# Performance work log

Measured on AMD Instinct MI355X. Metric: run time of the kernel, lower is better.

The kernel has to match this reference:

```python
import jax, jax.numpy as jnp
import numpy as np

N = 50000      # num_nodes
E = 800000     # num_edges (before self loops)
EMB = 128      # emb_dim
GH = 64        # gcn_hidden
TD = 4         # temporal_dim
B = 64         # batch of sequences
T = 200        # max sequence length
H = 128        # lstm_hidden (per direction)
IN_DIM = 2 + EMB + TD


def lstm_scan(x_tbi, w_ih, w_hh, b_ih, b_hh):
    """x_tbi: [T, B, I] -> hidden states [T, B, H]. PyTorch gate order i,f,g,o."""
    Bsz = x_tbi.shape[1]
    Hh = w_hh.shape[1]

    def step(carry, xt):
        h, c = carry
        g = xt @ w_ih.T + h @ w_hh.T + b_ih + b_hh
        i, f, gg, o = jnp.split(g, 4, axis=-1)
        c = jax.nn.sigmoid(f) * c + jax.nn.sigmoid(i) * jnp.tanh(gg)
        h = jax.nn.sigmoid(o) * jnp.tanh(c)
        return (h, c), h

    init = (jnp.zeros((Bsz, Hh), x_tbi.dtype), jnp.zeros((Bsz, Hh), x_tbi.dtype))
    _, hs = jax.lax.scan(step, init, x_tbi)
    return hs


def gcn_layer(x, W, b, src, dst, ew):
    """PyG GCNConv: linear -> symmetric-norm gather/scatter-add -> bias.
    (self loops already appended to src/dst/ew by caller)"""
    h = x @ W  # [N, out]
    deg = jax.ops.segment_sum(ew, dst, num_segments=N)
    dinv = jnp.where(deg > 0, jax.lax.rsqrt(deg), 0.0)
    norm = dinv[src] * ew * dinv[dst]            # [E+N]
    msg = h[src] * norm[:, None]                  # gather + scale
    return jax.ops.segment_sum(msg, dst, num_segments=N) + b


def setup_inputs() -> dict:
    key = jax.random.key(0)
    ks = jax.random.split(key, 16)
    s = 0.02
    return {
        'x_coords': jax.random.normal(ks[0], (N, 2), jnp.float32),
        'temporal_features': jax.random.uniform(ks[1], (N, TD), jnp.float32, -1.0, 1.0),
        'edge_index': jax.random.randint(ks[2], (2, E), 0, N),
        'edge_weight': jnp.ones((E,), jnp.float32),
        'seq': jax.random.randint(ks[3], (B, T), 0, N),
        'lengths': jax.random.randint(ks[4], (B,), 1, T + 1),
        'node_emb': jax.random.normal(ks[5], (N, EMB), jnp.float32) * s,
        'gcn1_w': jax.random.normal(ks[6], (IN_DIM, GH), jnp.float32) * s,
        'gcn1_b': jnp.zeros((GH,), jnp.float32),
        'gcn2_w': jax.random.normal(ks[7], (GH, EMB), jnp.float32) * s,
        'gcn2_b': jnp.zeros((EMB,), jnp.float32),
        'w_ih_f': jax.random.normal(ks[8], (4 * H, EMB), jnp.float32) * s,
        'w_hh_f': jax.random.normal(ks[9], (4 * H, H), jnp.float32) * s,
        'b_ih_f': jnp.zeros((4 * H,), jnp.float32),
        'b_hh_f': jnp.zeros((4 * H,), jnp.float32),
        'w_ih_b': jax.random.normal(ks[10], (4 * H, EMB), jnp.float32) * s,
        'w_hh_b': jax.random.normal(ks[11], (4 * H, H), jnp.float32) * s,
        'b_ih_b': jnp.zeros((4 * H,), jnp.float32),
        'b_hh_b': jnp.zeros((4 * H,), jnp.float32),
        'attn_w': jax.random.normal(ks[12], (2 * H,), jnp.float32) * s,
        'attn_b': jnp.zeros((), jnp.float32),
        'fc_w': jax.random.normal(ks[13], (2 * H, N), jnp.float32) * s,
        'fc_b': jnp.zeros((N,), jnp.float32),
    }


def reference(x_coords, temporal_features, edge_index, edge_weight, seq, lengths,
              node_emb, gcn1_w, gcn1_b, gcn2_w, gcn2_b,
              w_ih_f, w_hh_f, b_ih_f, b_hh_f,
              w_ih_b, w_hh_b, b_ih_b, b_hh_b,
              attn_w, attn_b, fc_w, fc_b):
    # --- GCN with self loops (PyG add_self_loops=True, fill_value=1) ---
    loop = jnp.arange(N)
    src = jnp.concatenate([edge_index[0], loop])
    dst = jnp.concatenate([edge_index[1], loop])
    ew = jnp.concatenate([edge_weight, jnp.ones((N,), edge_weight.dtype)])

    x = jnp.concatenate([x_coords, node_emb, temporal_features], axis=1)  # [N, 134]
    z = jax.nn.relu(gcn_layer(x, gcn1_w, gcn1_b, src, dst, ew))
    z = gcn_layer(z, gcn2_w, gcn2_b, src, dst, ew)  # dropout = identity (eval)

    # --- sequence embedding + BiLSTM ---
    seq_emb = z[seq]                                  # [B, T, EMB]
    h_f = lstm_scan(seq_emb.transpose(1, 0, 2), w_ih_f, w_hh_f, b_ih_f, b_hh_f)
    h_f = h_f.transpose(1, 0, 2)                      # [B, T, H]

    # backward direction: reverse each sequence within its valid length
    t = jnp.arange(T)
    valid = t[None, :] < lengths[:, None]             # [B, T]
    rev_idx = jnp.where(valid, lengths[:, None] - 1 - t[None, :], t[None, :])
    x_rev = jnp.take_along_axis(seq_emb, rev_idx[:, :, None], axis=1)
    h_b = lstm_scan(x_rev.transpose(1, 0, 2), w_ih_b, w_hh_b, b_ih_b, b_hh_b)
    h_b = jnp.take_along_axis(h_b.transpose(1, 0, 2), rev_idx[:, :, None], axis=1)

    lstm_out = jnp.concatenate([h_f, h_b], axis=-1)   # [B, T, 2H]

    # --- masked attention pooling ---
    scores = lstm_out @ attn_w + attn_b               # [B, T]
    scores = jnp.where(valid, scores, -jnp.inf)
    aw = jax.nn.softmax(scores, axis=1)
    context = jnp.einsum('bt,btd->bd', aw, lstm_out)  # [B, 2H]

    return context @ fc_w + fc_b                      # [B, N]
```

## Files before the change

kernel.cpp:

```cpp
#include <hip/hip_runtime.h>
#include <math.h>

#define NN 50000
#define NE 800000
#define EMB 128
#define GH 64
#define BB 64
#define TT 200
#define HH 128
#define G4 512
#define IND 134

__device__ __forceinline__ float sigf(float x) { return 1.0f / (1.0f + __expf(-x)); }
__device__ __forceinline__ float tanhf_(float x) { return 1.0f - 2.0f / (__expf(2.0f * x) + 1.0f); }
__device__ __forceinline__ void fma4(float4& a, float s, const float4 w) {
    a.x += s * w.x; a.y += s * w.y; a.z += s * w.z; a.w += s * w.w;
}

__global__ void hist_kernel(const int* __restrict__ ei, const float* __restrict__ ew,
                            int* __restrict__ cnt, float* __restrict__ degw) {
    int e = blockIdx.x * 256 + threadIdx.x;
    if (e >= NE) return;
    int d = ei[NE + e];
    atomicAdd(&cnt[d], 1);
    atomicAdd(&degw[d], ew[e]);
}

__global__ void dinv_kernel(const float* __restrict__ degw, float* __restrict__ dinv) {
    int n = blockIdx.x * 256 + threadIdx.x;
    if (n >= NN) return;
    dinv[n] = rsqrtf(degw[n] + 1.0f);
}

__global__ __launch_bounds__(1024) void scan1_kernel(const int* __restrict__ cnt,
                                                     int* __restrict__ rs, int* __restrict__ partials) {
    __shared__ int s[1024];
    int gid = blockIdx.x * 1024 + threadIdx.x;
    int v = (gid < NN) ? cnt[gid] : 0;
    s[threadIdx.x] = v;
    __syncthreads();
    for (int off = 1; off < 1024; off <<= 1) {
        int add = (threadIdx.x >= (unsigned)off) ? s[threadIdx.x - off] : 0;
        __syncthreads();
        s[threadIdx.x] += add;
        __syncthreads();
    }
    if (gid < NN) rs[gid] = s[threadIdx.x] - v;
    if (threadIdx.x == 1023) partials[blockIdx.x] = s[1023];
}

__global__ void scan2_kernel(int* __restrict__ partials, int nblk) {
    if (threadIdx.x == 0) {
        int acc = 0;
        for (int i = 0; i < nblk; ++i) { int v = partials[i]; partials[i] = acc; acc += v; }
    }
}

__global__ __launch_bounds__(1024) void scan3_kernel(const int* __restrict__ partials,
                                                     int* __restrict__ rs, int* __restrict__ cursor) {
    int gid = blockIdx.x * 1024 + threadIdx.x;
    if (gid < NN) {
        int v = rs[gid] + partials[gid >> 10];
        rs[gid] = v;
        cursor[gid] = v;
    }
    if (gid == 0) rs[NN] = NE;
}

__global__ void fill_kernel(const int* __restrict__ ei, const float* __restrict__ ew,
                            const float* __restrict__ dinv, int* __restrict__ cursor,
                            int* __restrict__ ssrc, float* __restrict__ sw) {
    int e = blockIdx.x * 256 + threadIdx.x;
    if (e >= NE) return;
    int s = ei[e], d = ei[NE + e];
    int pos = atomicAdd(&cursor[d], 1);
    ssrc[pos] = s;
    sw[pos] = ew[e] * dinv[s] * dinv[d];
}

__global__ __launch_bounds__(256) void gemm1_kernel(const float* __restrict__ coords,
                                                    const float* __restrict__ temporal,
                                                    const float* __restrict__ emb,
                                                    const float* __restrict__ W1,
                                                    float* __restrict__ h1) {
    __shared__ __align__(16) float wl[IND][GH];
    for (int i = threadIdx.x; i < IND * GH / 4; i += 256)
        ((float4*)wl)[i] = ((const float4*)W1)[i];
    __syncthreads();
    int n = blockIdx.x * 256 + threadIdx.x;
    if (n >= NN) return;
    float4 acc[16];
    float c0 = coords[2 * n], c1 = coords[2 * n + 1];
#pragma unroll
    for (int j = 0; j < 16; ++j) {
        float4 wa = *(const float4*)&wl[0][j * 4];
        float4 wb = *(const float4*)&wl[1][j * 4];
        float4 a;
        a.x = c0 * wa.x + c1 * wb.x; a.y = c0 * wa.y + c1 * wb.y;
        a.z = c0 * wa.z + c1 * wb.z; a.w = c0 * wa.w + c1 * wb.w;
        acc[j] = a;
    }
    const float4* er = (const float4*)(emb + (size_t)n * EMB);
#pragma unroll 2
    for (int k4 = 0; k4 < 32; ++k4) {
        float4 v = er[k4];
        int k = 2 + k4 * 4;
#pragma unroll
        for (int j = 0; j < 16; ++j) {
            fma4(acc[j], v.x, *(const float4*)&wl[k][j * 4]);
            fma4(acc[j], v.y, *(const float4*)&wl[k + 1][j * 4]);
            fma4(acc[j], v.z, *(const float4*)&wl[k + 2][j * 4]);
            fma4(acc[j], v.w, *(const float4*)&wl[k + 3][j * 4]);
        }
    }
    float t0 = temporal[4 * n], t1 = temporal[4 * n + 1], t2 = temporal[4 * n + 2], t3 = temporal[4 * n + 3];
#pragma unroll
    for (int j = 0; j < 16; ++j) {
        fma4(acc[j], t0, *(const float4*)&wl[130][j * 4]);
        fma4(acc[j], t1, *(const float4*)&wl[131][j * 4]);
        fma4(acc[j], t2, *(const float4*)&wl[132][j * 4]);
        fma4(acc[j], t3, *(const float4*)&wl[133][j * 4]);
        *(float4*)&h1[(size_t)n * GH + j * 4] = acc[j];
    }
}

__global__ __launch_bounds__(256) void agg_kernel(const float* __restrict__ hin,
                                                  const int* __restrict__ rs,
                                                  const int* __restrict__ ssrc,
                                                  const float* __restrict__ sw,
                                                  const float* __restrict__ dinv,
                                                  const float* __restrict__ bias, int relu,
                                                  float* __restrict__ hout) {
    int lane = threadIdx.x & 63;
    int wid = threadIdx.x >> 6;
    int n = blockIdx.x * 4 + wid;
    if (n >= NN) return;
    float dv = dinv[n];
    float acc = hin[(size_t)n * GH + lane] * (dv * dv);
    int i = rs[n], e1 = rs[n + 1];
    for (; i + 3 < e1; i += 4) {
        int s0 = ssrc[i], s1 = ssrc[i + 1], s2 = ssrc[i + 2], s3 = ssrc[i + 3];
        float w0 = sw[i], w1 = sw[i + 1], w2 = sw[i + 2], w3 = sw[i + 3];
        float a0 = hin[(size_t)s0 * GH + lane];
        float a1 = hin[(size_t)s1 * GH + lane];
        float a2 = hin[(size_t)s2 * GH + lane];
        float a3 = hin[(size_t)s3 * GH + lane];
        acc += a0 * w0 + a1 * w1 + a2 * w2 + a3 * w3;
    }
    for (; i < e1; ++i) acc += hin[(size_t)ssrc[i] * GH + lane] * sw[i];
    if (bias) acc += bias[lane];
    if (relu) acc = fmaxf(acc, 0.0f);
    hout[(size_t)n * GH + lane] = acc;
}

__global__ __launch_bounds__(256) void gemm2_kernel(const float* __restrict__ a2,
                                                    const float* __restrict__ W2,
                                                    const float* __restrict__ b2,
                                                    float* __restrict__ z2) {
    __shared__ __align__(16) float wl[GH][64];
    int j0 = blockIdx.y * 64;
    for (int i = threadIdx.x; i < GH * 16; i += 256) {
        int k = i >> 4, j4 = i & 15;
        *(float4*)&wl[k][j4 * 4] = *(const float4*)&W2[(size_t)k * EMB + j0 + j4 * 4];
    }
    __syncthreads();
    int n = blockIdx.x * 256 + threadIdx.x;
    if (n >= NN) return;
    float4 acc[16];
#pragma unroll
    for (int j = 0; j < 16; ++j) acc[j] = *(const float4*)&b2[j0 + j * 4];
    const float4* ar = (const float4*)(a2 + (size_t)n * GH);
#pragma unroll 2
    for (int k4 = 0; k4 < 16; ++k4) {
        float4 v = ar[k4];
        int k = k4 * 4;
#pragma unroll
        for (int j = 0; j < 16; ++j) {
            fma4(acc[j], v.x, *(const float4*)&wl[k][j * 4]);
            fma4(acc[j], v.y, *(const float4*)&wl[k + 1][j * 4]);
            fma4(acc[j], v.z, *(const float4*)&wl[k + 2][j * 4]);
            fma4(acc[j], v.w, *(const float4*)&wl[k + 3][j * 4]);
        }
    }
#pragma unroll
    for (int j = 0; j < 16; ++j)
        *(float4*)&z2[(size_t)n * EMB + j0 + j * 4] = acc[j];
}

__global__ void gather_kernel(const int* __restrict__ seq, const float* __restrict__ z2,
                              float* __restrict__ se) {
    int idx = blockIdx.x * 256 + threadIdx.x;
    if (idx >= BB * TT * 32) return;
    int r = idx >> 5, q = idx & 31;
    int node = seq[r];
    ((float4*)se)[(size_t)r * 32 + q] = ((const float4*)z2)[(size_t)node * 32 + q];
}

__global__ __launch_bounds__(256) void pregemm_kernel(const float* __restrict__ se,
                                                      const float* __restrict__ w_ih_f,
                                                      const float* __restrict__ w_ih_b,
                                                      const float* __restrict__ b_ih_f,
                                                      const float* __restrict__ b_hh_f,
                                                      const float* __restrict__ b_ih_b,
                                                      const float* __restrict__ b_hh_b,
                                                      const int* __restrict__ lengths,
                                                      float* __restrict__ xpf,
                                                      float* __restrict__ xpb) {
    int dir = blockIdx.z;
    const float* w_ih = dir ? w_ih_b : w_ih_f;
    int u0 = blockIdx.y * 64;
    __shared__ __align__(16) float wl[64][EMB];
    __shared__ float bs[64];
    {
        const float4* src = (const float4*)(w_ih + (size_t)u0 * EMB);
        for (int i = threadIdx.x; i < 64 * EMB / 4; i += 256) ((float4*)wl)[i] = src[i];
        if (threadIdx.x < 64) {
            int u = u0 + threadIdx.x;
            bs[threadIdx.x] = dir ? (b_ih_b[u] + b_hh_b[u]) : (b_ih_f[u] + b_hh_f[u]);
        }
    }
    __syncthreads();
    int m = blockIdx.x * 256 + threadIdx.x;
    if (m >= TT * BB) return;
    int t = m >> 6, b = m & 63;
    int tsrc = t;
    if (dir) {
        int len = lengths[b];
        if (t >= len) return;
        tsrc = len - 1 - t;
    }
    const float4* row = (const float4*)(se + ((size_t)b * TT + tsrc) * EMB);
    float accs[64];
#pragma unroll
    for (int j = 0; j < 64; ++j) accs[j] = bs[j];
#pragma unroll 2
    for (int k4 = 0; k4 < 32; ++k4) {
        float4 xv = row[k4];
#pragma unroll
        for (int j = 0; j < 64; ++j) {
            float4 wv = *(const float4*)&wl[j][k4 * 4];
            accs[j] += xv.x * wv.x + xv.y * wv.y + xv.z * wv.z + xv.w * wv.w;
        }
    }
    float* xp = dir ? xpb : xpf;
#pragma unroll
    for (int j4 = 0; j4 < 16; ++j4) {
        float4 o = make_float4(accs[j4 * 4], accs[j4 * 4 + 1], accs[j4 * 4 + 2], accs[j4 * 4 + 3]);
        *(float4*)&xp[(size_t)m * G4 + u0 + j4 * 4] = o;
    }
}

#define LSTM_LW(i) float4 W##i = wr[i]; \
    asm volatile("" : "+v"(W##i.x), "+v"(W##i.y), "+v"(W##i.z), "+v"(W##i.w));
#define LSTM_FMA(i) { float4 hv = h4[i]; \
    a0 += W##i.x * hv.x; a1 += W##i.y * hv.y; a2 += W##i.z * hv.z; a3 += W##i.w * hv.w; }

__global__ __launch_bounds__(512, 1) void lstm_kernel(const float* __restrict__ xpf,
                                                      const float* __restrict__ xpb,
                                                      const float* __restrict__ w_hh_f,
                                                      const float* __restrict__ w_hh_b,
                                                      const int* __restrict__ lengths,
                                                      float* __restrict__ hfo,
                                                      float* __restrict__ hbo) {
    int chain = blockIdx.x;
    int dir = chain & 1, b = chain >> 1;
    const float* w_hh = dir ? w_hh_b : w_hh_f;
    const float* xp = dir ? xpb : xpf;
    float* ho = dir ? hbo : hfo;
    int tid = threadIdx.x;
    int u = tid >> 2, g = tid & 3;
    int len = lengths[b];

    const float4* wr = (const float4*)(w_hh + (size_t)(g * HH + u) * HH);
    LSTM_LW(0) LSTM_LW(1) LSTM_LW(2) LSTM_LW(3) LSTM_LW(4) LSTM_LW(5) LSTM_LW(6) LSTM_LW(7)
    LSTM_LW(8) LSTM_LW(9) LSTM_LW(10) LSTM_LW(11) LSTM_LW(12) LSTM_LW(13) LSTM_LW(14) LSTM_LW(15)
    LSTM_LW(16) LSTM_LW(17) LSTM_LW(18) LSTM_LW(19) LSTM_LW(20) LSTM_LW(21) LSTM_LW(22) LSTM_LW(23)
    LSTM_LW(24) LSTM_LW(25) LSTM_LW(26) LSTM_LW(27) LSTM_LW(28) LSTM_LW(29) LSTM_LW(30) LSTM_LW(31)

    __shared__ __align__(16) float hl[2][HH];
    if (tid < HH) hl[0][tid] = 0.0f;
    __syncthreads();

    const float* xpt = xp + (size_t)b * G4 + g * HH + u;
    float cst = 0.0f;
    float xcur = xpt[0];
    for (int t = 0; t < len; ++t) {
        float xnext = (t + 1 < len) ? xpt[(size_t)(t + 1) * BB * G4] : 0.0f;
        const float4* h4 = (const float4*)hl[t & 1];
        float a0 = 0.0f, a1 = 0.0f, a2 = 0.0f, a3 = 0.0f;
        LSTM_FMA(0) LSTM_FMA(1) LSTM_FMA(2) LSTM_FMA(3) LSTM_FMA(4) LSTM_FMA(5) LSTM_FMA(6) LSTM_FMA(7)
        LSTM_FMA(8) LSTM_FMA(9) LSTM_FMA(10) LSTM_FMA(11) LSTM_FMA(12) LSTM_FMA(13) LSTM_FMA(14) LSTM_FMA(15)
        LSTM_FMA(16) LSTM_FMA(17) LSTM_FMA(18) LSTM_FMA(19) LSTM_FMA(20) LSTM_FMA(21) LSTM_FMA(22) LSTM_FMA(23)
        LSTM_FMA(24) LSTM_FMA(25) LSTM_FMA(26) LSTM_FMA(27) LSTM_FMA(28) LSTM_FMA(29) LSTM_FMA(30) LSTM_FMA(31)
        float acc = ((a0 + a1) + (a2 + a3)) + xcur;
        float a_own = (g == 2) ? tanhf_(acc) : sigf(acc);
        float sb = __shfl_xor(a_own, 1, 64);
        float sc = __shfl_xor(a_own, 2, 64);
        float sd = __shfl_xor(sb, 2, 64);
        float si = (g == 0) ? a_own : (g == 1) ? sb : (g == 2) ? sc : sd;
        float sf = (g == 0) ? sb : (g == 1) ? a_own : (g == 2) ? sd : sc;
        float sg = (g == 0) ? sc : (g == 1) ? sd : (g == 2) ? a_own : sb;
        float so = (g == 0) ? sd : (g == 1) ? sc : (g == 2) ? sb : a_own;
        cst = sf * cst + si * sg;
        float h = so * tanhf_(cst);
        if (g == 0) {
            hl[(t + 1) & 1][u] = h;
            int tt = dir ? (len - 1 - t) : t;
            ho[((size_t)b * TT + tt) * HH + u] = h;
        }
        __syncthreads();
        xcur = xnext;
    }
}

__global__ __launch_bounds__(256) void attn_kernel(const float* __restrict__ hf,
                                                   const float* __restrict__ hb,
                                                   const float* __restrict__ attn_w,
                                                   const float* __restrict__ attn_b,
                                                   const int* __restrict__ lengths,
                                                   float* __restrict__ ctx) {
    int b = blockIdx.x;
    int tid = threadIdx.x;
    int len = lengths[b];
    __shared__ __align__(16) float wl[256];
    __shared__ float pl[256];
    __shared__ float red[256];
    wl[tid] = attn_w[tid];
    __syncthreads();
    float sc = -3.0e38f;
    if (tid < len) {
        const float4* rf = (const float4*)(hf + ((size_t)b * TT + tid) * HH);
        const float4* rb = (const float4*)(hb + ((size_t)b * TT + tid) * HH);
        const float4* w4 = (const float4*)wl;
        float s = attn_b[0];
        for (int k4 = 0; k4 < 32; ++k4) {
            float4 a = rf[k4], ww = w4[k4];
            s += a.x * ww.x + a.y * ww.y + a.z * ww.z + a.w * ww.w;
        }
        for (int k4 = 0; k4 < 32; ++k4) {
            float4 a = rb[k4], ww = w4[32 + k4];
            s += a.x * ww.x + a.y * ww.y + a.z * ww.z + a.w * ww.w;
        }
        sc = s;
    }
    red[tid] = sc;
    __syncthreads();
    for (int off = 128; off > 0; off >>= 1) {
        if (tid < off) red[tid] = fmaxf(red[tid], red[tid + off]);
        __syncthreads();
    }
    float mx = red[0];
    __syncthreads();
    float e = (tid < len) ? __expf(sc - mx) : 0.0f;
    red[tid] = e;
    __syncthreads();
    for (int off = 128; off > 0; off >>= 1) {
        if (tid < off) red[tid] += red[tid + off];
        __syncthreads();
    }
    float inv = 1.0f / red[0];
    pl[tid] = e * inv;
    __syncthreads();
    float acc = 0.0f;
    const float* basep = (tid < HH) ? (hf + (size_t)b * TT * HH + tid)
                                    : (hb + (size_t)b * TT * HH + (tid - HH));
#pragma unroll 4
    for (int t = 0; t < len; ++t) acc += pl[t] * basep[(size_t)t * HH];
    ctx[(size_t)b * 256 + tid] = acc;
}

__global__ __launch_bounds__(256) void fc_kernel(const float* __restrict__ ctx,
                                                 const float* __restrict__ fc_w,
                                                 const float* __restrict__ fc_b,
                                                 float* __restrict__ out) {
    __shared__ __align__(16) float cl[64][256];
    for (int i = threadIdx.x; i < 64 * 256 / 4; i += 256)
        ((float4*)cl)[i] = ((const float4*)ctx)[i];
    __syncthreads();
    int nb = threadIdx.x & 63;
    int bq = threadIdx.x >> 6;
    int n = blockIdx.x * 64 + nb;
    if (n >= NN) return;
    float acc[16];
#pragma unroll
    for (int i = 0; i < 16; ++i) acc[i] = 0.0f;
#pragma unroll 2
    for (int k4 = 0; k4 < 64; ++k4) {
        int k = k4 * 4;
        float w0 = fc_w[(size_t)k * NN + n];
        float w1 = fc_w[(size_t)(k + 1) * NN + n];
        float w2 = fc_w[(size_t)(k + 2) * NN + n];
        float w3 = fc_w[(size_t)(k + 3) * NN + n];
#pragma unroll
        for (int i = 0; i < 16; ++i) {
            float4 cv = *(const float4*)&cl[bq * 16 + i][k];
            acc[i] += cv.x * w0 + cv.y * w1 + cv.z * w2 + cv.w * w3;
        }
    }
    float fb = fc_b[n];
#pragma unroll
    for (int i = 0; i < 16; ++i)
        out[(size_t)(bq * 16 + i) * NN + n] = acc[i] + fb;
}

extern "C" void kernel_launch(void* const* d_in, const int* in_sizes, int n_in,
                              void* d_out, int out_size, void* d_ws, size_t ws_size,
                              hipStream_t stream) {
    const float* x_coords   = (const float*)d_in[0];
    const float* temporal   = (const float*)d_in[1];
    const int*   edge_index = (const int*)d_in[2];
    const float* edge_w     = (const float*)d_in[3];
    const int*   seq        = (const int*)d_in[4];
    const int*   lengths    = (const int*)d_in[5];
    const float* node_emb   = (const float*)d_in[6];
    const float* gcn1_w     = (const float*)d_in[7];
    const float* gcn1_b     = (const float*)d_in[8];
    const float* gcn2_w     = (const float*)d_in[9];
    const float* gcn2_b     = (const float*)d_in[10];
    const float* w_ih_f     = (const float*)d_in[11];
    const float* w_hh_f     = (const float*)d_in[12];
    const float* b_ih_f     = (const float*)d_in[13];
    const float* b_hh_f     = (const float*)d_in[14];
    const float* w_ih_b     = (const float*)d_in[15];
    const float* w_hh_b     = (const float*)d_in[16];
    const float* b_ih_b     = (const float*)d_in[17];
    const float* b_hh_b     = (const float*)d_in[18];
    const float* attn_w     = (const float*)d_in[19];
    const float* attn_b     = (const float*)d_in[20];
    const float* fc_w       = (const float*)d_in[21];
    const float* fc_b       = (const float*)d_in[22];
    float* out = (float*)d_out;

    char* base = (char*)d_ws;
    size_t off = 0;
    auto alloc = [&](size_t nbytes) -> void* {
        void* p = base + off;
        off = (off + nbytes + 255) & ~(size_t)255;
        return p;
    };
    int*   cnt     = (int*)alloc((size_t)2 * NN * 4);
    float* degw    = (float*)(cnt + NN);
    float* dinv    = (float*)alloc((size_t)NN * 4);
    int*   rs      = (int*)alloc(((size_t)NN + 1) * 4);
    int*   cursor  = (int*)alloc((size_t)NN * 4);
    int*   partials= (int*)alloc(64 * 4);
    int*   ssrc    = (int*)alloc((size_t)NE * 4);
    float* sw      = (float*)alloc((size_t)NE * 4);
    float* h1      = (float*)alloc((size_t)NN * GH * 4);
    float* z1      = (float*)alloc((size_t)NN * GH * 4);
    float* a2      = h1;
    float* z2      = (float*)alloc((size_t)NN * EMB * 4);
    float* se      = (float*)alloc((size_t)BB * TT * EMB * 4);
    float* xpf     = (float*)alloc((size_t)TT * BB * G4 * 4);
    float* xpb     = (float*)alloc((size_t)TT * BB * G4 * 4);
    float* hfo     = (float*)alloc((size_t)BB * TT * HH * 4);
    float* hbo     = (float*)alloc((size_t)BB * TT * HH * 4);
    float* ctx     = (float*)alloc((size_t)BB * 256 * 4);
    (void)ws_size; (void)in_sizes; (void)n_in; (void)out_size;

    hipMemsetAsync(cnt, 0, (size_t)2 * NN * 4, stream);

    hist_kernel<<<(NE + 255) / 256, 256, 0, stream>>>(edge_index, edge_w, cnt, degw);
    dinv_kernel<<<(NN + 255) / 256, 256, 0, stream>>>(degw, dinv);
    const int nblk = (NN + 1023) / 1024;
    scan1_kernel<<<nblk, 1024, 0, stream>>>(cnt, rs, partials);
    scan2_kernel<<<1, 64, 0, stream>>>(partials, nblk);
    scan3_kernel<<<nblk, 1024, 0, stream>>>(partials, rs, cursor);
    fill_kernel<<<(NE + 255) / 256, 256, 0, stream>>>(edge_index, edge_w, dinv, cursor, ssrc, sw);

    gemm1_kernel<<<(NN + 255) / 256, 256, 0, stream>>>(x_coords, temporal, node_emb, gcn1_w, h1);
    agg_kernel<<<(NN + 3) / 4, 256, 0, stream>>>(h1, rs, ssrc, sw, dinv, gcn1_b, 1, z1);
    agg_kernel<<<(NN + 3) / 4, 256, 0, stream>>>(z1, rs, ssrc, sw, dinv, (const float*)nullptr, 0, a2);
    gemm2_kernel<<<dim3((NN + 255) / 256, 2), 256, 0, stream>>>(a2, gcn2_w, gcn2_b, z2);

    gather_kernel<<<(BB * TT * 32 + 255) / 256, 256, 0, stream>>>(seq, z2, se);
    pregemm_kernel<<<dim3(TT * BB / 256, 8, 2), 256, 0, stream>>>(
        se, w_ih_f, w_ih_b, b_ih_f, b_hh_f, b_ih_b, b_hh_b, lengths, xpf, xpb);
    lstm_kernel<<<BB * 2, 512, 0, stream>>>(xpf, xpb, w_hh_f, w_hh_b, lengths, hfo, hbo);
    attn_kernel<<<BB, 256, 0, stream>>>(hfo, hbo, attn_w, attn_b, lengths, ctx);
    fc_kernel<<<(NN + 63) / 64, 256, 0, stream>>>(ctx, fc_w, fc_b, out);
}
```

Baseline: 692.7 us.

## Split LSTM recurrent matvec over two thread halves and broadcast h via readlane

The recurrent kernel now uses 1024 threads per chain, with each half holding 64 of the 128 weight columns in registers, which halves the serial dot-product length per thread. The hidden-state vector is no longer read from LDS as float4 per step. Each lane loads one element and the values are broadcast with readlane. The two halves combine through a shared partial-sum buffer, which adds an extra barrier per timestep and leaves the second half idle during the gate nonlinearities.

```diff
diff --git a/kernel.cpp b/kernel.cpp
--- a/kernel.cpp
+++ b/kernel.cpp
@@ -15,6 +15,9 @@
 __device__ __forceinline__ float tanhf_(float x) { return 1.0f - 2.0f / (__expf(2.0f * x) + 1.0f); }
 __device__ __forceinline__ void fma4(float4& a, float s, const float4 w) {
     a.x += s * w.x; a.y += s * w.y; a.z += s * w.z; a.w += s * w.w;
+}
+__device__ __forceinline__ float rlf(float x, int k) {
+    return __int_as_float(__builtin_amdgcn_readlane(__float_as_int(x), k));
 }
 
 __global__ void hist_kernel(const int* __restrict__ ei, const float* __restrict__ ew,
@@ -252,61 +255,75 @@
 
 #define LSTM_LW(i) float4 W##i = wr[i]; \
     asm volatile("" : "+v"(W##i.x), "+v"(W##i.y), "+v"(W##i.z), "+v"(W##i.w));
-#define LSTM_FMA(i) { float4 hv = h4[i]; \
-    a0 += W##i.x * hv.x; a1 += W##i.y * hv.y; a2 += W##i.z * hv.z; a3 += W##i.w * hv.w; }
-
-__global__ __launch_bounds__(512, 1) void lstm_kernel(const float* __restrict__ xpf,
-                                                      const float* __restrict__ xpb,
-                                                      const float* __restrict__ w_hh_f,
-                                                      const float* __restrict__ w_hh_b,
-                                                      const int* __restrict__ lengths,
-                                                      float* __restrict__ hfo,
-                                                      float* __restrict__ hbo) {
+#define LSTM_RLFMA(i) { \
+    float s0 = rlf(hfrag, 4*i+0); a0 += s0 * W##i.x; \
+    float s1 = rlf(hfrag, 4*i+1); a1 += s1 * W##i.y; \
+    float s2 = rlf(hfrag, 4*i+2); a2 += s2 * W##i.z; \
+    float s3 = rlf(hfrag, 4*i+3); a3 += s3 * W##i.w; }
+
+__global__ __launch_bounds__(1024, 4) void lstm_kernel(const float* __restrict__ xpf,
+                                                       const float* __restrict__ xpb,
+                                                       const float* __restrict__ w_hh_f,
+                                                       const float* __restrict__ w_hh_b,
+                                                       const int* __restrict__ lengths,
+                                                       float* __restrict__ hfo,
+                                                       float* __restrict__ hbo) {
     int chain = blockIdx.x;
     int dir = chain & 1, b = chain >> 1;
     const float* w_hh = dir ? w_hh_b : w_hh_f;
     const float* xp = dir ? xpb : xpf;
     float* ho = dir ? hbo : hfo;
     int tid = threadIdx.x;
-    int u = tid >> 2, g = tid & 3;
+    int wv = tid >> 6;
+    int lam = tid & 63;
+    int p = wv >> 3;
+    int wj = wv & 7;
+    int j = wj * 64 + lam;
+    int g = lam & 3;
+    int u = j >> 2;
+    int r = g * HH + u;
     int len = lengths[b];
 
-    const float4* wr = (const float4*)(w_hh + (size_t)(g * HH + u) * HH);
+    const float4* wr = (const float4*)(w_hh + (size_t)r * HH + p * 64);
     LSTM_LW(0) LSTM_LW(1) LSTM_LW(2) LSTM_LW(3) LSTM_LW(4) LSTM_LW(5) LSTM_LW(6) LSTM_LW(7)
     LSTM_LW(8) LSTM_LW(9) LSTM_LW(10) LSTM_LW(11) LSTM_LW(12) LSTM_LW(13) LSTM_LW(14) LSTM_LW(15)
-    LSTM_LW(16) LSTM_LW(17) LSTM_LW(18) LSTM_LW(19) LSTM_LW(20) LSTM_LW(21) LSTM_LW(22) LSTM_LW(23)
-    LSTM_LW(24) LSTM_LW(25) LSTM_LW(26) LSTM_LW(27) LSTM_LW(28) LSTM_LW(29) LSTM_LW(30) LSTM_LW(31)
-
-    __shared__ __align__(16) float hl[2][HH];
-    if (tid < HH) hl[0][tid] = 0.0f;
-    __syncthreads();
-
-    const float* xpt = xp + (size_t)b * G4 + g * HH + u;
+
+    __shared__ float hl[HH];
+    __shared__ float part[G4];
+    if (tid < HH) hl[tid] = 0.0f;
+    __syncthreads();
+
+    const float* xpt = xp + (size_t)b * G4 + r;
     float cst = 0.0f;
-    float xcur = xpt[0];
+    float xcur = (p == 0) ? xpt[0] : 0.0f;
     for (int t = 0; t < len; ++t) {
-        float xnext = (t + 1 < len) ? xpt[(size_t)(t + 1) * BB * G4] : 0.0f;
-        const float4* h4 = (const float4*)hl[t & 1];
+        float hfrag = hl[(p << 6) + lam];
+        float xnext = (p == 0 && t + 1 < len) ? xpt[(size_t)(t + 1) * (BB * G4)] : 0.0f;
         float a0 = 0.0f, a1 = 0.0f, a2 = 0.0f, a3 = 0.0f;
-        LSTM_FMA(0) LSTM_FMA(1) LSTM_FMA(2) LSTM_FMA(3) LSTM_FMA(4) LSTM_FMA(5) LSTM_FMA(6) LSTM_FMA(7)
-        LSTM_FMA(8) LSTM_FMA(9) LSTM_FMA(10) LSTM_FMA(11) LSTM_FMA(12) LSTM_FMA(13) LSTM_FMA(14) LSTM_FMA(15)
-        LSTM_FMA(16) LSTM_FMA(17) LSTM_FMA(18) LSTM_FMA(19) LSTM_FMA(20) LSTM_FMA(21) LSTM_FMA(22) LSTM_FMA(23)
-        LSTM_FMA(24) LSTM_FMA(25) LSTM_FMA(26) LSTM_FMA(27) LSTM_FMA(28) LSTM_FMA(29) LSTM_FMA(30) LSTM_FMA(31)
-        float acc = ((a0 + a1) + (a2 + a3)) + xcur;
-        float a_own = (g == 2) ? tanhf_(acc) : sigf(acc);
-        float sb = __shfl_xor(a_own, 1, 64);
-        float sc = __shfl_xor(a_own, 2, 64);
-        float sd = __shfl_xor(sb, 2, 64);
-        float si = (g == 0) ? a_own : (g == 1) ? sb : (g == 2) ? sc : sd;
-        float sf = (g == 0) ? sb : (g == 1) ? a_own : (g == 2) ? sd : sc;
-        float sg = (g == 0) ? sc : (g == 1) ? sd : (g == 2) ? a_own : sb;
-        float so = (g == 0) ? sd : (g == 1) ? sc : (g == 2) ? sb : a_own;
-        cst = sf * cst + si * sg;
-        float h = so * tanhf_(cst);
-        if (g == 0) {
-            hl[(t + 1) & 1][u] = h;
-            int tt = dir ? (len - 1 - t) : t;
-            ho[((size_t)b * TT + tt) * HH + u] = h;
+        LSTM_RLFMA(0) LSTM_RLFMA(1) LSTM_RLFMA(2) LSTM_RLFMA(3)
+        LSTM_RLFMA(4) LSTM_RLFMA(5) LSTM_RLFMA(6) LSTM_RLFMA(7)
+        LSTM_RLFMA(8) LSTM_RLFMA(9) LSTM_RLFMA(10) LSTM_RLFMA(11)
+        LSTM_RLFMA(12) LSTM_RLFMA(13) LSTM_RLFMA(14) LSTM_RLFMA(15)
+        float accp = (a0 + a1) + (a2 + a3);
+        if (p) part[j] = accp;
+        __syncthreads();
+        if (p == 0) {
+            float acc = accp + part[j] + xcur;
+            float a_own = (g == 2) ? tanhf_(acc) : sigf(acc);
+            float sb = __shfl_xor(a_own, 1, 64);
+            float sc = __shfl_xor(a_own, 2, 64);
+            float sd = __shfl_xor(sb, 2, 64);
+            float si = (g == 0) ? a_own : (g == 1) ? sb : (g == 2) ? sc : sd;
+            float sf = (g == 0) ? sb : (g == 1) ? a_own : (g == 2) ? sd : sc;
+            float sg = (g == 0) ? sc : (g == 1) ? sd : (g == 2) ? a_own : sb;
+            float so = (g == 0) ? sd : (g == 1) ? sc : (g == 2) ? sb : a_own;
+            cst = sf * cst + si * sg;
+            float h = so * tanhf_(cst);
+            if (g == 0) {
+                hl[u] = h;
+                int tt = dir ? (len - 1 - t) : t;
+                ho[((size_t)b * TT + tt) * HH + u] = h;
+            }
         }
         __syncthreads();
         xcur = xnext;
@@ -476,7 +493,7 @@
     gather_kernel<<<(BB * TT * 32 + 255) / 256, 256, 0, stream>>>(seq, z2, se);
     pregemm_kernel<<<dim3(TT * BB / 256, 8, 2), 256, 0, stream>>>(
         se, w_ih_f, w_ih_b, b_ih_f, b_hh_f, b_ih_b, b_hh_b, lengths, xpf, xpb);
-    lstm_kernel<<<BB * 2, 512, 0, stream>>>(xpf, xpb, w_hh_f, w_hh_b, lengths, hfo, hbo);
+    lstm_kernel<<<BB * 2, 1024, 0, stream>>>(xpf, xpb, w_hh_f, w_hh_b, lengths, hfo, hbo);
     attn_kernel<<<BB, 256, 0, stream>>>(hfo, hbo, attn_w, attn_b, lengths, ctx);
     fc_kernel<<<(NN + 63) / 64, 256, 0, stream>>>(ctx, fc_w, fc_b, out);
 }
```

Result: slower. 773.8 us (+11.7%).
